# Performance work log

Hardware: AMD Instinct MI355X
Metric: run time of the kernel (lower is better)

The kernel has to match this reference:

```python
import jax, jax.numpy as jnp
import numpy as np

N_NODES = 100000
N_EDGES = 1600000
D = 64
N_GRAPHS = 64


def setup_inputs() -> dict:
    key = jax.random.key(0)
    ks = jax.random.split(key, 8)
    x = jax.random.normal(ks[0], (N_NODES, D), dtype=jnp.float32)
    edge_index = jax.random.randint(ks[1], (2, N_EDGES), 0, N_NODES)
    batch = jnp.sort(jax.random.randint(ks[2], (N_NODES,), 0, N_GRAPHS))
    edge_weight = jax.random.uniform(ks[3], (N_EDGES,), dtype=jnp.float32)
    s = 1.0 / np.sqrt(D)
    W1 = jax.random.normal(ks[4], (D, D), dtype=jnp.float32) * s
    b1 = jnp.zeros((D,), dtype=jnp.float32)
    W2 = jax.random.normal(ks[5], (D, D), dtype=jnp.float32) * s
    b2 = jnp.zeros((D,), dtype=jnp.float32)
    return {"x": x, "edge_index": edge_index, "batch": batch,
            "edge_weight": edge_weight, "W1": W1, "b1": b1, "W2": W2, "b2": b2}


def reference(x, edge_index, batch, edge_weight, W1, b1, W2, b2):
    # --- GCN normalization with self-loops (PyG gcn_norm, fill_value=1) ---
    loop = jnp.arange(N_NODES)
    src = jnp.concatenate([edge_index[0], loop])
    dst = jnp.concatenate([edge_index[1], loop])
    ew = jnp.concatenate([edge_weight, jnp.ones((N_NODES,), x.dtype)])
    deg = jax.ops.segment_sum(ew, dst, num_segments=N_NODES)
    dinv = jnp.where(deg > 0, jax.lax.rsqrt(deg), 0.0)
    norm = dinv[src] * ew * dinv[dst]  # [E+N]

    def gcn_relu(h, W, b):
        h = h @ W                                   # [N, D]
        msg = h[src] * norm[:, None]                # gather + weight messages
        agg = jax.ops.segment_sum(msg, dst, num_segments=N_NODES)
        return jax.nn.relu(agg + b)

    h = gcn_relu(x, W1, b1)
    h = gcn_relu(h, W2, b2)

    # --- global mean pool over graphs ---
    sums = jax.ops.segment_sum(h, batch, num_segments=N_GRAPHS)
    counts = jax.ops.segment_sum(jnp.ones((N_NODES, 1), h.dtype), batch,
                                 num_segments=N_GRAPHS)
    return sums / jnp.maximum(counts, 1.0)
```

## Files before the change

### kernel.cpp

```cpp
#include <hip/hip_runtime.h>

#define N_NODES 100000
#define N_EDGES 1600000
#define D 64
#define N_GRAPHS 64
#define NBLK ((N_NODES + 255) / 256)
#define WTS 68

__global__ void k_init(float* __restrict__ deg, int* __restrict__ cnt,
                       float* __restrict__ out) {
    int i = blockIdx.x * blockDim.x + threadIdx.x;
    if (i < N_NODES) { deg[i] = 1.0f; cnt[i] = 0; }
    if (i < N_GRAPHS * D) out[i] = 0.0f;
}

__global__ void k_count_deg(const int* __restrict__ dst, const float* __restrict__ ew,
                            float* __restrict__ deg, int* __restrict__ cnt) {
    int e = blockIdx.x * blockDim.x + threadIdx.x;
    if (e < N_EDGES) {
        int d = dst[e];
        atomicAdd(&deg[d], ew[e]);
        atomicAdd(&cnt[d], 1);
    }
}

__global__ void k_dinv(float* __restrict__ deg) {
    int i = blockIdx.x * blockDim.x + threadIdx.x;
    if (i < N_NODES) {
        float d = deg[i];
        deg[i] = d > 0.f ? rsqrtf(d) : 0.f;
    }
}

__global__ void k_scan1(const int* __restrict__ cnt, int* __restrict__ partial,
                        int* __restrict__ bsums) {
    int t = threadIdx.x, b = blockIdx.x, i = b * 256 + t;
    int v = (i < N_NODES) ? cnt[i] : 0;
    int incl = v;
    int lane = t & 63;
#pragma unroll
    for (int off = 1; off < 64; off <<= 1) {
        int u = __shfl_up(incl, off);
        if (lane >= off) incl += u;
    }
    __shared__ int wsum[4];
    int w = t >> 6;
    if (lane == 63) wsum[w] = incl;
    __syncthreads();
    int add = 0;
    for (int k = 0; k < w; ++k) add += wsum[k];
    incl += add;
    if (i < N_NODES) partial[i] = incl;
    if (t == 255) bsums[b] = incl;
}

__global__ void k_scan2(int* __restrict__ bsums) {
    __shared__ int s[512];
    int t = threadIdx.x;
    s[t] = (t < NBLK) ? bsums[t] : 0;
    __syncthreads();
    for (int off = 1; off < 512; off <<= 1) {
        int u = (t >= off) ? s[t - off] : 0;
        __syncthreads();
        s[t] += u;
        __syncthreads();
    }
    if (t < NBLK) bsums[t] = (t == 0) ? 0 : s[t - 1];
}

__global__ void k_scan3(const int* __restrict__ partial, const int* __restrict__ cnt,
                        const int* __restrict__ bsums, int* __restrict__ rowptr,
                        int* __restrict__ cursor) {
    int i = blockIdx.x * 256 + threadIdx.x;
    if (i < N_NODES) {
        int excl = partial[i] - cnt[i] + bsums[blockIdx.x];
        rowptr[i] = excl;
        cursor[i] = excl;
    }
}

__global__ void k_scatter(const int* __restrict__ src, const int* __restrict__ dst,
                          const float* __restrict__ ew, const float* __restrict__ dinv,
                          int* __restrict__ cursor, float2* __restrict__ csr) {
    int e = blockIdx.x * blockDim.x + threadIdx.x;
    if (e < N_EDGES) {
        int s = src[e];
        int d = dst[e];
        float nrm = dinv[s] * ew[e] * dinv[d];
        int pos = atomicAdd(&cursor[d], 1);
        csr[pos] = make_float2(__int_as_float(s), nrm);
    }
}


#define EPASS(U)                                                              \
    {                                                                         \
        int  jj = j + (U);                                                    \
        int  ii = st + (jj < dgm1 ? jj : dgm1);                               \
        float2 e = csr[ii];                                                   \
        float  w = (jj < dg) ? e.y : 0.0f;                                    \
        int    s = __builtin_amdgcn_readfirstlane(__float_as_int(e.x));       \
        float  v = in[s * D + lane];                                          \
        acc = fmaf(v, w, acc);                                                \
    }

template <int LAYER>
__global__ __launch_bounds__(1024) void k_layer(
        const float* __restrict__ in, const float* __restrict__ W,
        const float* __restrict__ bias, const float* __restrict__ dinv,
        const int* __restrict__ rowptr, const int* __restrict__ cnt,
        const float2* __restrict__ csr, const int* __restrict__ batch,
        float* __restrict__ outp) {
    __shared__ float WTs[D * WTS];
    __shared__ float aw[16][D];
    __shared__ float bs[D];

    {
        int t = threadIdx.x;
#pragma unroll
        for (int i = 0; i < 4; ++i) {
            int idx = t + i * 1024;
            int k = idx >> 6, c = idx & 63;
            WTs[c * WTS + k] = W[idx];
        }
        if (t < D) bs[t] = bias[t];
    }
    __syncthreads();

    const int lane = threadIdx.x & 63;
    const int wid  = threadIdx.x >> 6;
    float* awm = aw[wid];
    const float bl = bs[lane];

    int gw = (blockIdx.x * blockDim.x + threadIdx.x) >> 6;
    const int tw = (gridDim.x * blockDim.x) >> 6;

    for (int row = gw; row < N_NODES; row += tw) {
        const int st = __builtin_amdgcn_readfirstlane(rowptr[row]);
        const int dg = __builtin_amdgcn_readfirstlane(cnt[row]);
        const int dgm1 = dg - 1;
        float di = dinv[row];
        float acc = in[row * D + lane] * (di * di);

        const int passes = (dg + 7) >> 3;
        for (int p = 0; p < passes; ++p) {
            const int j = p * 8;
            int  jj0 = j + 0, jj1 = j + 1, jj2 = j + 2, jj3 = j + 3;
            int  jj4 = j + 4, jj5 = j + 5, jj6 = j + 6, jj7 = j + 7;
            float2 e0 = csr[st + (jj0 < dgm1 ? jj0 : dgm1)];
            float2 e1 = csr[st + (jj1 < dgm1 ? jj1 : dgm1)];
            float2 e2 = csr[st + (jj2 < dgm1 ? jj2 : dgm1)];
            float2 e3 = csr[st + (jj3 < dgm1 ? jj3 : dgm1)];
            float2 e4 = csr[st + (jj4 < dgm1 ? jj4 : dgm1)];
            float2 e5 = csr[st + (jj5 < dgm1 ? jj5 : dgm1)];
            float2 e6 = csr[st + (jj6 < dgm1 ? jj6 : dgm1)];
            float2 e7 = csr[st + (jj7 < dgm1 ? jj7 : dgm1)];
            float w0 = (jj0 < dg) ? e0.y : 0.f;
            float w1 = (jj1 < dg) ? e1.y : 0.f;
            float w2 = (jj2 < dg) ? e2.y : 0.f;
            float w3 = (jj3 < dg) ? e3.y : 0.f;
            float w4 = (jj4 < dg) ? e4.y : 0.f;
            float w5 = (jj5 < dg) ? e5.y : 0.f;
            float w6 = (jj6 < dg) ? e6.y : 0.f;
            float w7 = (jj7 < dg) ? e7.y : 0.f;
            int s0 = __builtin_amdgcn_readfirstlane(__float_as_int(e0.x));
            int s1 = __builtin_amdgcn_readfirstlane(__float_as_int(e1.x));
            int s2 = __builtin_amdgcn_readfirstlane(__float_as_int(e2.x));
            int s3 = __builtin_amdgcn_readfirstlane(__float_as_int(e3.x));
            int s4 = __builtin_amdgcn_readfirstlane(__float_as_int(e4.x));
            int s5 = __builtin_amdgcn_readfirstlane(__float_as_int(e5.x));
            int s6 = __builtin_amdgcn_readfirstlane(__float_as_int(e6.x));
            int s7 = __builtin_amdgcn_readfirstlane(__float_as_int(e7.x));
            float v0 = in[s0 * D + lane];
            float v1 = in[s1 * D + lane];
            float v2 = in[s2 * D + lane];
            float v3 = in[s3 * D + lane];
            float v4 = in[s4 * D + lane];
            float v5 = in[s5 * D + lane];
            float v6 = in[s6 * D + lane];
            float v7 = in[s7 * D + lane];
            acc = fmaf(v0, w0, acc);
            acc = fmaf(v1, w1, acc);
            acc = fmaf(v2, w2, acc);
            acc = fmaf(v3, w3, acc);
            acc = fmaf(v4, w4, acc);
            acc = fmaf(v5, w5, acc);
            acc = fmaf(v6, w6, acc);
            acc = fmaf(v7, w7, acc);
        }

        awm[lane] = acc;
        float r0 = 0.f, r1 = 0.f, r2 = 0.f, r3 = 0.f;
#pragma unroll
        for (int t = 0; t < 16; ++t) {
            float4 a = *(const float4*)&awm[t * 4];
            float4 w = *(const float4*)&WTs[lane * WTS + t * 4];
            r0 = fmaf(a.x, w.x, r0);
            r1 = fmaf(a.y, w.y, r1);
            r2 = fmaf(a.z, w.z, r2);
            r3 = fmaf(a.w, w.w, r3);
        }
        float r = fmaxf((r0 + r1) + (r2 + r3) + bl, 0.f);

        if (LAYER == 1) {
            outp[row * D + lane] = r;
        } else {
            atomicAdd(&outp[batch[row] * D + lane], r);
        }
    }
}

__global__ void k_finalize(float* __restrict__ out, const int* __restrict__ batch) {
    int g = blockIdx.x;
    int lane = threadIdx.x;
    int lo = 0, hi = N_NODES;
    while (lo < hi) { int m = (lo + hi) >> 1; if (batch[m] < g) lo = m + 1; else hi = m; }
    int start = lo;
    hi = N_NODES;
    while (lo < hi) { int m = (lo + hi) >> 1; if (batch[m] < g + 1) lo = m + 1; else hi = m; }
    float c = (float)(lo - start);
    out[g * D + lane] /= fmaxf(c, 1.0f);
}

extern "C" void kernel_launch(void* const* d_in, const int* in_sizes, int n_in,
                              void* d_out, int out_size, void* d_ws, size_t ws_size,
                              hipStream_t stream) {
    const float* x     = (const float*)d_in[0];
    const int*   ei    = (const int*)d_in[1];
    const int*   src   = ei;
    const int*   dst   = ei + N_EDGES;
    const int*   batch = (const int*)d_in[2];
    const float* ew    = (const float*)d_in[3];
    const float* W1    = (const float*)d_in[4];
    const float* b1    = (const float*)d_in[5];
    const float* W2    = (const float*)d_in[6];
    const float* b2    = (const float*)d_in[7];
    float* out = (float*)d_out;

    char* ws = (char*)d_ws;
    float*  bufA   = (float*)(ws);
    float2* csr    = (float2*)(ws + 25600000);
    float*  deg    = (float*)(ws + 38400000);
    int*    cnt    = (int*)(ws + 38800000);
    int*    rowptr = (int*)(ws + 39200000);
    int*    cursor = (int*)(ws + 39600000);
    int*    bsums  = (int*)(ws + 40000000);

    k_init<<<NBLK, 256, 0, stream>>>(deg, cnt, out);
    k_count_deg<<<(N_EDGES + 255) / 256, 256, 0, stream>>>(dst, ew, deg, cnt);
    k_dinv<<<NBLK, 256, 0, stream>>>(deg);
    k_scan1<<<NBLK, 256, 0, stream>>>(cnt, rowptr, bsums);
    k_scan2<<<1, 512, 0, stream>>>(bsums);
    k_scan3<<<NBLK, 256, 0, stream>>>(rowptr, cnt, bsums, rowptr, cursor);
    k_scatter<<<(N_EDGES + 255) / 256, 256, 0, stream>>>(src, dst, ew, deg, cursor, csr);

    k_layer<1><<<512, 1024, 0, stream>>>(x, W1, b1, deg, rowptr, cnt, csr, batch, bufA);
    k_layer<2><<<512, 1024, 0, stream>>>(bufA, W2, b2, deg, rowptr, cnt, csr, batch, out);
    k_finalize<<<N_GRAPHS, D, 0, stream>>>(out, batch);
}
```

Before: 519.9 us.

## Store node features in fp16 for gathers and fold dinv into scan

Converts the input features to half precision in a new pre-pass and stores the layer-1 output in fp16, which halves the bytes moved by the random neighbour gathers in both aggregation layers. The separate init and dinv kernels are removed: buffers are zeroed with memsets, and rsqrt(deg+1) is computed inside the first scan kernel. The trade-offs are fp16 rounding of the activations and an extra conversion pass over x. The gather loads are still 2-byte per-lane loads, so per-request efficiency may be limited.

```diff
diff --git a/kernel.cpp b/kernel.cpp
--- a/kernel.cpp
+++ b/kernel.cpp
@@ -1,4 +1,5 @@
 #include <hip/hip_runtime.h>
+#include <hip/hip_fp16.h>
 
 #define N_NODES 100000
 #define N_EDGES 1600000
@@ -6,13 +7,6 @@
 #define N_GRAPHS 64
 #define NBLK ((N_NODES + 255) / 256)
 #define WTS 68
-
-__global__ void k_init(float* __restrict__ deg, int* __restrict__ cnt,
-                       float* __restrict__ out) {
-    int i = blockIdx.x * blockDim.x + threadIdx.x;
-    if (i < N_NODES) { deg[i] = 1.0f; cnt[i] = 0; }
-    if (i < N_GRAPHS * D) out[i] = 0.0f;
-}
 
 __global__ void k_count_deg(const int* __restrict__ dst, const float* __restrict__ ew,
                             float* __restrict__ deg, int* __restrict__ cnt) {
@@ -24,17 +18,13 @@
     }
 }
 
-__global__ void k_dinv(float* __restrict__ deg) {
-    int i = blockIdx.x * blockDim.x + threadIdx.x;
+__global__ void k_scan1(const int* __restrict__ cnt, int* __restrict__ partial,
+                        int* __restrict__ bsums, float* __restrict__ deg) {
+    int t = threadIdx.x, b = blockIdx.x, i = b * 256 + t;
     if (i < N_NODES) {
         float d = deg[i];
-        deg[i] = d > 0.f ? rsqrtf(d) : 0.f;
-    }
-}
-
-__global__ void k_scan1(const int* __restrict__ cnt, int* __restrict__ partial,
-                        int* __restrict__ bsums) {
-    int t = threadIdx.x, b = blockIdx.x, i = b * 256 + t;
+        deg[i] = rsqrtf(d + 1.0f);
+    }
     int v = (i < N_NODES) ? cnt[i] : 0;
     int incl = v;
     int lane = t & 63;
@@ -92,25 +82,26 @@
     }
 }
 
-
-#define EPASS(U)                                                              \
-    {                                                                         \
-        int  jj = j + (U);                                                    \
-        int  ii = st + (jj < dgm1 ? jj : dgm1);                               \
-        float2 e = csr[ii];                                                   \
-        float  w = (jj < dg) ? e.y : 0.0f;                                    \
-        int    s = __builtin_amdgcn_readfirstlane(__float_as_int(e.x));       \
-        float  v = in[s * D + lane];                                          \
-        acc = fmaf(v, w, acc);                                                \
-    }
+__global__ void k_half(const float* __restrict__ x, __half* __restrict__ xh) {
+    int i = blockIdx.x * blockDim.x + threadIdx.x;
+    const int total = N_NODES * D / 4;
+    const int stride = gridDim.x * blockDim.x;
+    const float4* x4 = (const float4*)x;
+    __half2* xh2 = (__half2*)xh;
+    for (; i < total; i += stride) {
+        float4 v = x4[i];
+        xh2[2 * i + 0] = __floats2half2_rn(v.x, v.y);
+        xh2[2 * i + 1] = __floats2half2_rn(v.z, v.w);
+    }
+}
 
 template <int LAYER>
 __global__ __launch_bounds__(1024) void k_layer(
-        const float* __restrict__ in, const float* __restrict__ W,
+        const __half* __restrict__ in, const float* __restrict__ W,
         const float* __restrict__ bias, const float* __restrict__ dinv,
         const int* __restrict__ rowptr, const int* __restrict__ cnt,
         const float2* __restrict__ csr, const int* __restrict__ batch,
-        float* __restrict__ outp) {
+        __half* __restrict__ outh, float* __restrict__ outf) {
     __shared__ float WTs[D * WTS];
     __shared__ float aw[16][D];
     __shared__ float bs[D];
@@ -140,7 +131,7 @@
         const int dg = __builtin_amdgcn_readfirstlane(cnt[row]);
         const int dgm1 = dg - 1;
         float di = dinv[row];
-        float acc = in[row * D + lane] * (di * di);
+        float acc = __half2float(in[row * D + lane]) * (di * di);
 
         const int passes = (dg + 7) >> 3;
         for (int p = 0; p < passes; ++p) {
@@ -171,14 +162,14 @@
             int s5 = __builtin_amdgcn_readfirstlane(__float_as_int(e5.x));
             int s6 = __builtin_amdgcn_readfirstlane(__float_as_int(e6.x));
             int s7 = __builtin_amdgcn_readfirstlane(__float_as_int(e7.x));
-            float v0 = in[s0 * D + lane];
-            float v1 = in[s1 * D + lane];
-            float v2 = in[s2 * D + lane];
-            float v3 = in[s3 * D + lane];
-            float v4 = in[s4 * D + lane];
-            float v5 = in[s5 * D + lane];
-            float v6 = in[s6 * D + lane];
-            float v7 = in[s7 * D + lane];
+            float v0 = __half2float(in[s0 * D + lane]);
+            float v1 = __half2float(in[s1 * D + lane]);
+            float v2 = __half2float(in[s2 * D + lane]);
+            float v3 = __half2float(in[s3 * D + lane]);
+            float v4 = __half2float(in[s4 * D + lane]);
+            float v5 = __half2float(in[s5 * D + lane]);
+            float v6 = __half2float(in[s6 * D + lane]);
+            float v7 = __half2float(in[s7 * D + lane]);
             acc = fmaf(v0, w0, acc);
             acc = fmaf(v1, w1, acc);
             acc = fmaf(v2, w2, acc);
@@ -203,9 +194,9 @@
         float r = fmaxf((r0 + r1) + (r2 + r3) + bl, 0.f);
 
         if (LAYER == 1) {
-            outp[row * D + lane] = r;
+            outh[row * D + lane] = __float2half_rn(r);
         } else {
-            atomicAdd(&outp[batch[row] * D + lane], r);
+            atomicAdd(&outf[batch[row] * D + lane], r);
         }
     }
 }
@@ -238,7 +229,8 @@
     float* out = (float*)d_out;
 
     char* ws = (char*)d_ws;
-    float*  bufA   = (float*)(ws);
+    __half* xh     = (__half*)(ws);
+    __half* hh     = (__half*)(ws + 12800000);
     float2* csr    = (float2*)(ws + 25600000);
     float*  deg    = (float*)(ws + 38400000);
     int*    cnt    = (int*)(ws + 38800000);
@@ -246,15 +238,18 @@
     int*    cursor = (int*)(ws + 39600000);
     int*    bsums  = (int*)(ws + 40000000);
 
-    k_init<<<NBLK, 256, 0, stream>>>(deg, cnt, out);
+    hipMemsetAsync(deg, 0, N_NODES * sizeof(float), stream);
+    hipMemsetAsync(cnt, 0, N_NODES * sizeof(int), stream);
+    hipMemsetAsync(out, 0, N_GRAPHS * D * sizeof(float), stream);
+
+    k_half<<<1024, 256, 0, stream>>>(x, xh);
     k_count_deg<<<(N_EDGES + 255) / 256, 256, 0, stream>>>(dst, ew, deg, cnt);
-    k_dinv<<<NBLK, 256, 0, stream>>>(deg);
-    k_scan1<<<NBLK, 256, 0, stream>>>(cnt, rowptr, bsums);
+    k_scan1<<<NBLK, 256, 0, stream>>>(cnt, rowptr, bsums, deg);
     k_scan2<<<1, 512, 0, stream>>>(bsums);
     k_scan3<<<NBLK, 256, 0, stream>>>(rowptr, cnt, bsums, rowptr, cursor);
     k_scatter<<<(N_EDGES + 255) / 256, 256, 0, stream>>>(src, dst, ew, deg, cursor, csr);
 
-    k_layer<1><<<512, 1024, 0, stream>>>(x, W1, b1, deg, rowptr, cnt, csr, batch, bufA);
-    k_layer<2><<<512, 1024, 0, stream>>>(bufA, W2, b2, deg, rowptr, cnt, csr, batch, out);
+    k_layer<1><<<512, 1024, 0, stream>>>(xh, W1, b1, deg, rowptr, cnt, csr, batch, hh, out);
+    k_layer<2><<<512, 1024, 0, stream>>>(hh, W2, b2, deg, rowptr, cnt, csr, batch, hh, out);
     k_finalize<<<N_GRAPHS, D, 0, stream>>>(out, batch);
 }
```

Result: faster. 466.6 us (-10.2%).
